# Kernel optimization log

Hardware: AMD Instinct MI355X
Metric: run time of the kernel (lower is better)

The kernel has to match this reference:

```python
import jax, jax.numpy as jnp
import numpy as np

B, T, L = 512, 512, 256
XC, SC, NZ, H, OC = 16, 8, 8, 128, 8
INFO = SC + NZ + 1   # 17: [y, zx, t] channels for the zy (past) encoder
CF = NZ + 1          # 9: [zx, t] channels for the future CDE control
W = 128              # CDEFunc MLP width (width_dfunc default)


def setup_inputs() -> dict:
    key = jax.random.key(0)
    ks = jax.random.split(key, 20)
    rn = lambda k, s: jax.random.normal(k, s, dtype=jnp.float32)
    sc = lambda fan: np.float32(1.0 / np.sqrt(fan))
    return dict(
        y_past=rn(ks[0], (B, L, SC)),
        t=jnp.arange(T, dtype=jnp.float32),
        coeffs_x=rn(ks[1], (B, T, XC)),
        input_length=L,
        zx_wih=rn(ks[2], (3 * H, XC + 1)) * sc(XC + 1),
        zx_whh=rn(ks[3], (3 * H, H)) * sc(H),
        zx_b=rn(ks[4], (3 * H,)) * sc(H),
        zx_bn=rn(ks[5], (H,)) * sc(H),
        zxl_w=rn(ks[6], (NZ, H)) * sc(H),
        zxl_b=rn(ks[7], (NZ,)) * sc(H),
        zy_wih=rn(ks[8], (3 * H, INFO)) * sc(INFO),
        zy_whh=rn(ks[9], (3 * H, H)) * sc(H),
        zy_b=rn(ks[10], (3 * H,)) * sc(H),
        zy_bn=rn(ks[11], (H,)) * sc(H),
        f_w1=rn(ks[12], (W, H)) * sc(H),
        f_b1=rn(ks[13], (W,)) * sc(H),
        f_w2=rn(ks[14], (W, W)) * sc(W),
        f_b2=rn(ks[15], (W,)) * sc(W),
        f_w3=rn(ks[16], (H * CF, W)) * sc(W),
        f_b3=rn(ks[17], (H * CF,)) * sc(W),
        r_w=rn(ks[18], (OC, H)) * sc(H),
        r_b=rn(ks[19], (OC,)) * sc(H),
    )


def _gru(xs, wih, whh, b, bn):
    # xs: (T, B, C). Equinox GRUCell math, batched over B.
    h0 = jnp.zeros((xs.shape[1], whh.shape[1]), xs.dtype)

    def step(h, x):
        i_r, i_z, i_n = jnp.split(x @ wih.T + b, 3, axis=-1)
        g_r, g_z, g_n = jnp.split(h @ whh.T, 3, axis=-1)
        r = jax.nn.sigmoid(i_r + g_r)
        z = jax.nn.sigmoid(i_z + g_z)
        n = jnp.tanh(i_n + r * (g_n + bn))
        hn = n + z * (h - n)  # == new + inp*(hidden-new) in eqx
        return hn, hn

    hT, hs = jax.lax.scan(step, h0, xs)
    return hT, hs


def reference(y_past, t, coeffs_x, input_length,
              zx_wih, zx_whh, zx_b, zx_bn, zxl_w, zxl_b,
              zy_wih, zy_whh, zy_b, zy_bn,
              f_w1, f_b1, f_w2, f_b2, f_w3, f_b3, r_w, r_b):
    Bsz = y_past.shape[0]
    tc = jnp.broadcast_to(t[None, :, None], (Bsz, t.shape[0], 1))
    # --- zx encoder (GRU over control path [X, t]; linear interp at knots == data) ---
    ctrl = jnp.concatenate([coeffs_x, tc], axis=-1)                 # (B,T,XC+1)
    _, hs = _gru(jnp.swapaxes(ctrl, 0, 1), zx_wih, zx_whh, zx_b, zx_bn)
    zx = jnp.swapaxes(hs, 0, 1) @ zxl_w.T + zxl_b                   # (B,T,NZ)
    Lp = input_length
    # --- zy encoder over past control [y, zx, t] (plan_option='full') ---
    ctrl_past = jnp.concatenate([y_past, zx[:, :Lp], tc[:, :Lp]], axis=-1)  # (B,L,INFO)
    zy_current, _ = _gru(jnp.swapaxes(ctrl_past, 0, 1), zy_wih, zy_whh, zy_b, zy_bn)  # (B,H)
    # --- future CDE: dz = f(z) @ dX with linear control X = [zx_future, t_future] ---
    ctrl_fut = jnp.concatenate([zx[:, Lp:], tc[:, Lp:]], axis=-1)   # (B,F,CF)
    dX = jnp.diff(ctrl_fut, axis=1)                                 # (B,F-1,CF)

    def vf(z):  # CDEFunc MLP: (B,H) -> (B,H,CF)
        h1 = jax.nn.softplus(z @ f_w1.T + f_b1)
        h2 = jax.nn.softplus(h1 @ f_w2.T + f_b2)
        o = jnp.tanh(h2 @ f_w3.T + f_b3)
        return o.reshape(z.shape[0], -1, CF)

    def rk4(z, dx):  # one RK4 step per knot interval (dX absorbs dt * slope)
        k1 = jnp.einsum('bhc,bc->bh', vf(z), dx)
        k2 = jnp.einsum('bhc,bc->bh', vf(z + 0.5 * k1), dx)
        k3 = jnp.einsum('bhc,bc->bh', vf(z + 0.5 * k2), dx)
        k4 = jnp.einsum('bhc,bc->bh', vf(z + k3), dx)
        zn = z + (k1 + 2.0 * k2 + 2.0 * k3 + k4) / 6.0
        return zn, zn

    _, zs = jax.lax.scan(rk4, zy_current, jnp.swapaxes(dX, 0, 1))   # (F-1,B,H)
    ys = jnp.concatenate([zy_current[None], zs], axis=0)            # (F,B,H) saveat ts
    y_hat = jnp.swapaxes(ys, 0, 1) @ r_w.T + r_b                    # (B,F,OC)
    return y_hat
```

## Files before the change

### kernel.cpp

```cpp
#include <hip/hip_runtime.h>

#define Bb 512
#define Tt 512
#define Ll 256
#define Ff 256
#define Hh 128
#define H3 384
#define NZ 8
#define XC 16
#define OC 8
#define CF 9
#define W3N 1152
#define BBt 2

__device__ __forceinline__ float sigm(float x){ return 1.0f/(1.0f+expf(-x)); }
__device__ __forceinline__ float softplus_(float x){
  return fmaxf(x, 0.0f) + log1pf(expf(-fabsf(x)));
}
__device__ __forceinline__ float tanh_fast(float x){
  float xc = fminf(fmaxf(x, -9.f), 9.f);
  float e = __expf(2.f*xc);
  return (e - 1.f)/(e + 1.f);
}
__device__ __forceinline__ float dot4(float4 w, float4 z){
  return w.x*z.x + w.y*z.y + w.z*z.z + w.w*z.w;
}
__device__ __forceinline__ int swz32(int i){ return i ^ ((i >> 3) & 3); }
__device__ __forceinline__ int swzf(int h){ return (((h >> 2) ^ ((h >> 5) & 3)) << 2) + (h & 3); }
__device__ __forceinline__ float red4(float p){
  int t;
  t = __builtin_amdgcn_mov_dpp(__builtin_bit_cast(int, p), 0xB1, 0xF, 0xF, true);
  p += __builtin_bit_cast(float, t);
  t = __builtin_amdgcn_mov_dpp(__builtin_bit_cast(int, p), 0x4E, 0xF, 0xF, true);
  p += __builtin_bit_cast(float, t);
  return p;
}
__device__ __forceinline__ float red8(float p){
  p = red4(p);
  int t = __builtin_amdgcn_ds_swizzle(__builtin_bit_cast(int, p), 0x101F);
  p += __builtin_bit_cast(float, t);
  return p;
}

__global__ __launch_bounds__(768) void gru_kernel(
    const float* __restrict__ xin, const float* __restrict__ zx_in,
    const float* __restrict__ tin,
    const float* __restrict__ wih, const float* __restrict__ whh,
    const float* __restrict__ bias, const float* __restrict__ bn,
    const float* __restrict__ zxlw, const float* __restrict__ zxlb,
    float* __restrict__ out_zx, float* __restrict__ out_h,
    int steps, int mode)
{
  const int b = blockIdx.x;
  const int tid = threadIdx.x;
  const int j = tid >> 1;
  const int half = tid & 1;

  float wi[17];
  #pragma unroll
  for (int c = 0; c < 17; c++) wi[c] = wih[j*17 + c];
  const float bj = bias[j];
  float4 wr[16];
  {
    const float4* p = reinterpret_cast<const float4*>(whh + (size_t)j*Hh + half*64);
    #pragma unroll
    for (int q = 0; q < 16; q++) wr[q] = p[q];
  }

  __shared__ __align__(16) float s_h[Hh];
  __shared__ float s_i[H3];
  __shared__ float s_g[H3];
  __shared__ float s_x[17];
  __shared__ float s_bn[Hh];
  __shared__ float s_zxlwT[NZ*Hh];
  __shared__ float s_zxlb[NZ];

  if (tid < Hh){ s_h[tid] = 0.0f; s_bn[tid] = bn[tid]; }
  if (mode == 0){
    for (int q2 = tid; q2 < NZ*Hh; q2 += 768){
      int o = q2 >> 7, rem = q2 & 127, m = rem >> 3, q = rem & 7;
      s_zxlwT[q*128 + o*16 + m] = zxlw[q2];
    }
    if (tid < NZ) s_zxlb[tid] = zxlb[tid];
  }

  float xreg = 0.f;
  if (tid < 17){
    if (mode == 0){
      xreg = (tid < 16) ? xin[(size_t)b*Tt*XC + tid] : tin[0];
    } else {
      if (tid < 8)       xreg = xin[(size_t)b*Ll*NZ + tid];
      else if (tid < 16) xreg = zx_in[(size_t)b*Tt*NZ + (tid - 8)];
      else               xreg = tin[0];
    }
  }
  __syncthreads();

  for (int t = 0; t < steps; t++){
    if (tid < 17) s_x[tid] = xreg;
    __syncthreads();
    float ai = bj;
    #pragma unroll
    for (int c = 0; c < 17; c++) ai += wi[c]*s_x[c];
    float g0=0.f, g1=0.f, g2=0.f, g3=0.f;
    {
      const float4* h4p = reinterpret_cast<const float4*>(&s_h[half*64]);
      #pragma unroll
      for (int q = 0; q < 16; q++){
        float4 w = wr[q];
        float4 h4 = h4p[q];
        g0 += w.x*h4.x; g1 += w.y*h4.y; g2 += w.z*h4.z; g3 += w.w*h4.w;
      }
    }
    float g = (g0+g1)+(g2+g3);
    g += __shfl_xor(g, 1, 64);
    if (half == 0){ s_i[j] = ai; s_g[j] = g; }
    if (tid < 17 && t + 1 < steps){
      const int tn = t + 1;
      if (mode == 0){
        xreg = (tid < 16) ? xin[(size_t)b*Tt*XC + (size_t)tn*XC + tid] : tin[tn];
      } else {
        if (tid < 8)       xreg = xin[(size_t)b*Ll*NZ + (size_t)tn*NZ + tid];
        else if (tid < 16) xreg = zx_in[(size_t)b*Tt*NZ + (size_t)tn*NZ + (tid - 8)];
        else               xreg = tin[tn];
      }
    }
    __syncthreads();
    if (tid < Hh){
      float r  = sigm(s_i[tid]       + s_g[tid]);
      float zz = sigm(s_i[Hh + tid]  + s_g[Hh + tid]);
      float n  = tanhf(s_i[2*Hh+tid] + r*(s_g[2*Hh+tid] + s_bn[tid]));
      s_h[tid] = n + zz*(s_h[tid] - n);
    }
    __syncthreads();
    if (mode == 0){
      if (tid < Hh){
        int m = tid & 15;
        const float4* hp = reinterpret_cast<const float4*>(&s_h[m*8]);
        float4 ha = hp[0], hb = hp[1];
        float p = s_zxlwT[0*128 + tid]*ha.x + s_zxlwT[1*128 + tid]*ha.y
                + s_zxlwT[2*128 + tid]*ha.z + s_zxlwT[3*128 + tid]*ha.w
                + s_zxlwT[4*128 + tid]*hb.x + s_zxlwT[5*128 + tid]*hb.y
                + s_zxlwT[6*128 + tid]*hb.z + s_zxlwT[7*128 + tid]*hb.w;
        p += __shfl_xor(p, 1, 64); p += __shfl_xor(p, 2, 64);
        p += __shfl_xor(p, 4, 64); p += __shfl_xor(p, 8, 64);
        if (m == 0)
          out_zx[(size_t)b*Tt*NZ + (size_t)t*NZ + (tid >> 4)] = s_zxlb[tid >> 4] + p;
      }
    }
  }
  if (mode == 1 && tid < Hh) out_h[b*Hh + tid] = s_h[tid];
}

__global__ __launch_bounds__(512)
__attribute__((amdgpu_waves_per_eu(2, 2)))
void cde_fp32_kernel(
    const float* __restrict__ zy_h, const float* __restrict__ zx,
    const float* __restrict__ tin,
    const float* __restrict__ fw1, const float* __restrict__ fb1,
    const float* __restrict__ fw2, const float* __restrict__ fb2,
    const float* __restrict__ fw3, const float* __restrict__ fb3,
    const float* __restrict__ rw,  const float* __restrict__ rb,
    float* __restrict__ yout)
{
  const int tid = threadIdx.x;
  const int c12 = tid >> 2;
  const int q4  = tid & 3;
  const int col64 = tid >> 3;
  const int e8    = tid & 7;
  const int bg = blockIdx.x * BBt;

  __shared__ __align__(16) float4 s_w1v[4096];
  __shared__ __align__(16) float4 s_w2v[4096];
  __shared__ __align__(16) float4 s_zinv[BBt][32];
  __shared__ __align__(16) float4 s_h1v[BBt][32];
  __shared__ __align__(16) float4 s_h2v[BBt][32];
  __shared__ float s_o[BBt][W3N];
  __shared__ float s_z[BBt][Hh];
  __shared__ float s_kacc[BBt][Hh];
  __shared__ float s_dx[BBt][CF];
  __shared__ float s_rw[OC*Hh];
  __shared__ float s_rb[OC];
  __shared__ float s_b3[W3N];

  float* zin_f0 = reinterpret_cast<float*>(&s_zinv[0][0]);
  float* zin_f1 = reinterpret_cast<float*>(&s_zinv[1][0]);
  float* h1_f0  = reinterpret_cast<float*>(&s_h1v[0][0]);
  float* h1_f1  = reinterpret_cast<float*>(&s_h1v[1][0]);
  float* h2_f0  = reinterpret_cast<float*>(&s_h2v[0][0]);
  float* h2_f1  = reinterpret_cast<float*>(&s_h2v[1][0]);

  for (int idx = tid; idx < Hh*32; idx += 512){
    int col = idx >> 5, jcol = idx & 31;
    int q = jcol >> 3, jj = jcol & 7;
    int dst = jj*512 + col*4 + q;
    s_w1v[dst] = reinterpret_cast<const float4*>(fw1)[idx];
    s_w2v[dst] = reinterpret_cast<const float4*>(fw2)[idx];
  }
  const float b1r = fb1[c12], b2r = fb2[c12];
  for (int idx = tid; idx < W3N; idx += 512) s_b3[idx] = fb3[idx];
  for (int idx = tid; idx < OC*Hh; idx += 512) s_rw[idx] = rw[idx];
  if (tid < OC) s_rb[tid] = rb[tid];
  if (tid < BBt*Hh){
    int b = tid >> 7, h = tid & 127;
    float zv = zy_h[(size_t)(bg + b)*Hh + h];
    s_z[b][h] = zv;
    (b == 0 ? zin_f0 : zin_f1)[swzf(h)] = zv;
  }
  __syncthreads();

  if (tid < 256){
    int b = tid >> 7, r = tid & 127, o = r >> 4, seg = r & 15;
    float p = 0.f;
    #pragma unroll
    for (int q = 0; q < 8; q++)
      p += s_z[b][seg*8 + q]*s_rw[o*Hh + seg*8 + q];
    p += __shfl_xor(p, 1, 64); p += __shfl_xor(p, 2, 64);
    p += __shfl_xor(p, 4, 64); p += __shfl_xor(p, 8, 64);
    if (seg == 0) yout[(size_t)(bg + b)*Ff*OC + o] = s_rb[o] + p;
  }

  const float* w3p = fw3 + (size_t)col64*Hh + e8*16;

  for (int i = 0; i < Ff - 1; i++){
    if (tid < BBt*CF){
      int b = tid/CF, c = tid%CF;
      float d;
      if (c < 8){
        const float* zp = zx + (size_t)(bg + b)*Tt*NZ + (size_t)(Ll + i)*NZ + c;
        d = zp[NZ] - zp[0];
      } else {
        d = tin[Ll + i + 1] - tin[Ll + i];
      }
      s_dx[b][c] = d;
    }
    __syncthreads();

    for (int st = 0; st < 4; st++){
      float4 A0, A1, A2, A3, B0, B1, B2, B3;
      {
        const float4* pA = reinterpret_cast<const float4*>(w3p);
        const float4* pB = reinterpret_cast<const float4*>(w3p + 8192);
        A0 = pA[0]; A1 = pA[1]; A2 = pA[2]; A3 = pA[3];
        B0 = pB[0]; B1 = pB[1]; B2 = pB[2]; B3 = pB[3];
      }
      {
        float p0 = 0.f, p1 = 0.f;
        #pragma unroll
        for (int jj = 0; jj < 8; jj++){
          float4 z0 = s_zinv[0][swz32(q4*8 + jj)];
          float4 z1 = s_zinv[1][swz32(q4*8 + jj)];
          float4 w = s_w1v[jj*512 + tid];
          p0 += dot4(w, z0); p1 += dot4(w, z1);
        }
        p0 = red4(p0); p1 = red4(p1);
        if (q4 == 0){
          h1_f0[swzf(c12)] = softplus_(b1r + p0);
          h1_f1[swzf(c12)] = softplus_(b1r + p1);
        }
      }
      __syncthreads();
      {
        float p0 = 0.f, p1 = 0.f;
        #pragma unroll
        for (int jj = 0; jj < 8; jj++){
          float4 z0 = s_h1v[0][swz32(q4*8 + jj)];
          float4 z1 = s_h1v[1][swz32(q4*8 + jj)];
          float4 w = s_w2v[jj*512 + tid];
          p0 += dot4(w, z0); p1 += dot4(w, z1);
        }
        p0 = red4(p0); p1 = red4(p1);
        if (q4 == 0){
          h2_f0[swzf(c12)] = softplus_(b2r + p0);
          h2_f1[swzf(c12)] = softplus_(b2r + p1);
        }
      }
      __syncthreads();
      {
        float4 h2a0 = s_h2v[0][swz32(e8*4 + 0)];
        float4 h2a1 = s_h2v[0][swz32(e8*4 + 1)];
        float4 h2a2 = s_h2v[0][swz32(e8*4 + 2)];
        float4 h2a3 = s_h2v[0][swz32(e8*4 + 3)];
        float4 h2b0 = s_h2v[1][swz32(e8*4 + 0)];
        float4 h2b1 = s_h2v[1][swz32(e8*4 + 1)];
        float4 h2b2 = s_h2v[1][swz32(e8*4 + 2)];
        float4 h2b3 = s_h2v[1][swz32(e8*4 + 3)];
        #pragma unroll 2
        for (int g = 0; g < 18; g++){
          float4 c0, c1, c2, c3;
          if ((g & 1) == 0){
            c0 = A0; c1 = A1; c2 = A2; c3 = A3;
            if (g + 2 < 18){
              const float4* pF = reinterpret_cast<const float4*>(w3p + (size_t)(g+2)*8192);
              A0 = pF[0]; A1 = pF[1]; A2 = pF[2]; A3 = pF[3];
            }
          } else {
            c0 = B0; c1 = B1; c2 = B2; c3 = B3;
            if (g + 2 < 18){
              const float4* pF = reinterpret_cast<const float4*>(w3p + (size_t)(g+2)*8192);
              B0 = pF[0]; B1 = pF[1]; B2 = pF[2]; B3 = pF[3];
            }
          }
          float p0 = dot4(c0, h2a0) + dot4(c1, h2a1) + dot4(c2, h2a2) + dot4(c3, h2a3);
          float p1 = dot4(c0, h2b0) + dot4(c1, h2b1) + dot4(c2, h2b2) + dot4(c3, h2b3);
          p0 = red8(p0); p1 = red8(p1);
          if (e8 == 0){
            int n = g*64 + col64;
            s_o[0][n] = s_b3[n] + p0;
            s_o[1][n] = s_b3[n] + p1;
          }
        }
      }
      __syncthreads();
      {
        int pr = tid >> 1, hf = tid & 1;
        int b = pr >> 7, h = pr & 127;
        const float* ob = &s_o[0][0] + b*W3N + h*CF;
        float kc = 0.f;
        #pragma unroll
        for (int jj = 0; jj < 4; jj++){
          int c = hf*4 + jj;
          kc += tanh_fast(ob[c]) * s_dx[b][c];
        }
        if (hf) kc += tanh_fast(ob[8]) * s_dx[b][8];
        kc += __shfl_xor(kc, 1, 64);
        if (hf == 0){
          float zv = s_z[b][h], zin;
          if      (st == 0){ s_kacc[b][h] = kc;        zin = zv + 0.5f*kc; }
          else if (st == 1){ s_kacc[b][h] += 2.f*kc;   zin = zv + 0.5f*kc; }
          else if (st == 2){ s_kacc[b][h] += 2.f*kc;   zin = zv + kc; }
          else { float zn = zv + (s_kacc[b][h] + kc)*(1.f/6.f); s_z[b][h] = zn; zin = zn; }
          (b == 0 ? zin_f0 : zin_f1)[swzf(h)] = zin;
        }
      }
      __syncthreads();
    }
    if (tid < 256){
      int b = tid >> 7, r = tid & 127, o = r >> 4, seg = r & 15;
      float p = 0.f;
      #pragma unroll
      for (int q = 0; q < 8; q++)
        p += s_z[b][seg*8 + q]*s_rw[o*Hh + seg*8 + q];
      p += __shfl_xor(p, 1, 64); p += __shfl_xor(p, 2, 64);
      p += __shfl_xor(p, 4, 64); p += __shfl_xor(p, 8, 64);
      if (seg == 0) yout[(size_t)(bg + b)*Ff*OC + (size_t)(i + 1)*OC + o] = s_rb[o] + p;
    }
  }
}

extern "C" void kernel_launch(void* const* d_in, const int* in_sizes, int n_in,
                              void* d_out, int out_size, void* d_ws, size_t ws_size,
                              hipStream_t stream)
{
  (void)in_sizes; (void)n_in; (void)out_size; (void)ws_size;
  const float* y_past = (const float*)d_in[0];
  const float* t_in   = (const float*)d_in[1];
  const float* coeffs = (const float*)d_in[2];
  const float* zx_wih = (const float*)d_in[4];
  const float* zx_whh = (const float*)d_in[5];
  const float* zx_b   = (const float*)d_in[6];
  const float* zx_bn  = (const float*)d_in[7];
  const float* zxl_w  = (const float*)d_in[8];
  const float* zxl_b  = (const float*)d_in[9];
  const float* zy_wih = (const float*)d_in[10];
  const float* zy_whh = (const float*)d_in[11];
  const float* zy_b   = (const float*)d_in[12];
  const float* zy_bn  = (const float*)d_in[13];
  const float* fw1 = (const float*)d_in[14];
  const float* fb1 = (const float*)d_in[15];
  const float* fw2 = (const float*)d_in[16];
  const float* fb2 = (const float*)d_in[17];
  const float* fw3 = (const float*)d_in[18];
  const float* fb3 = (const float*)d_in[19];
  const float* r_w = (const float*)d_in[20];
  const float* r_b = (const float*)d_in[21];

  float* ws = (float*)d_ws;
  float* zx_buf = ws;
  float* zy_buf = ws + (size_t)Bb*Tt*NZ;

  gru_kernel<<<Bb, 768, 0, stream>>>(coeffs, nullptr, t_in,
                                     zx_wih, zx_whh, zx_b, zx_bn,
                                     zxl_w, zxl_b, zx_buf, nullptr, Tt, 0);
  gru_kernel<<<Bb, 768, 0, stream>>>(y_past, zx_buf, t_in,
                                     zy_wih, zy_whh, zy_b, zy_bn,
                                     nullptr, nullptr, nullptr, zy_buf, Ll, 1);
  cde_fp32_kernel<<<Bb/BBt, 512, 0, stream>>>(zy_buf, zx_buf, t_in,
                                              fw1, fb1, fw2, fb2, fw3, fb3,
                                              r_w, r_b, (float*)d_out);
}
```

Measured before the change: 13.54 ms.

## Fuse zx and zy GRU encoders into one kernel and use fast transcendentals

Merges the two GRU launches into a single kernel per batch row. The zx projections for the past window stay in shared memory and feed the zy GRU directly, so they are no longer written to and re-read from global memory. Only the future part of zx still goes to the workspace. Sigmoid, tanh and softplus in the GRU and CDE MLP now use __expf/__logf-based fast versions, which cuts latency on the serial recurrence at some cost in accuracy. The fused kernel uses more shared memory (an extra 8 KB buffer).

Result: faster. 12.00 ms (-11.4%).

```diff
diff --git a/kernel.cpp b/kernel.cpp
--- a/kernel.cpp
+++ b/kernel.cpp
@@ -13,9 +13,10 @@
 #define W3N 1152
 #define BBt 2
 
-__device__ __forceinline__ float sigm(float x){ return 1.0f/(1.0f+expf(-x)); }
-__device__ __forceinline__ float softplus_(float x){
-  return fmaxf(x, 0.0f) + log1pf(expf(-fabsf(x)));
+__device__ __forceinline__ float sigm_fast(float x){ return 1.0f/(1.0f + __expf(-x)); }
+__device__ __forceinline__ float softplus_fast(float x){
+  float u = __expf(-fabsf(x));
+  return fmaxf(x, 0.0f) + __logf(1.0f + u);
 }
 __device__ __forceinline__ float tanh_fast(float x){
   float xc = fminf(fmaxf(x, -9.f), 9.f);
@@ -42,30 +43,20 @@
   return p;
 }
 
-__global__ __launch_bounds__(768) void gru_kernel(
-    const float* __restrict__ xin, const float* __restrict__ zx_in,
+__global__ __launch_bounds__(768) void gru_fused_kernel(
+    const float* __restrict__ coeffs, const float* __restrict__ y_past,
     const float* __restrict__ tin,
-    const float* __restrict__ wih, const float* __restrict__ whh,
-    const float* __restrict__ bias, const float* __restrict__ bn,
-    const float* __restrict__ zxlw, const float* __restrict__ zxlb,
-    float* __restrict__ out_zx, float* __restrict__ out_h,
-    int steps, int mode)
+    const float* __restrict__ zx_wih, const float* __restrict__ zx_whh,
+    const float* __restrict__ zx_b,   const float* __restrict__ zx_bn,
+    const float* __restrict__ zxlw,   const float* __restrict__ zxlb,
+    const float* __restrict__ zy_wih, const float* __restrict__ zy_whh,
+    const float* __restrict__ zy_b,   const float* __restrict__ zy_bn,
+    float* __restrict__ out_zx, float* __restrict__ out_h)
 {
   const int b = blockIdx.x;
   const int tid = threadIdx.x;
   const int j = tid >> 1;
   const int half = tid & 1;
-
-  float wi[17];
-  #pragma unroll
-  for (int c = 0; c < 17; c++) wi[c] = wih[j*17 + c];
-  const float bj = bias[j];
-  float4 wr[16];
-  {
-    const float4* p = reinterpret_cast<const float4*>(whh + (size_t)j*Hh + half*64);
-    #pragma unroll
-    for (int q = 0; q < 16; q++) wr[q] = p[q];
-  }
 
   __shared__ __align__(16) float s_h[Hh];
   __shared__ float s_i[H3];
@@ -74,66 +65,63 @@
   __shared__ float s_bn[Hh];
   __shared__ float s_zxlwT[NZ*Hh];
   __shared__ float s_zxlb[NZ];
-
-  if (tid < Hh){ s_h[tid] = 0.0f; s_bn[tid] = bn[tid]; }
-  if (mode == 0){
+  __shared__ float s_zxh[Ll][NZ];
+
+  {
+    float wi[17];
+    #pragma unroll
+    for (int c = 0; c < 17; c++) wi[c] = zx_wih[j*17 + c];
+    const float bj = zx_b[j];
+    float4 wr[16];
+    {
+      const float4* p = reinterpret_cast<const float4*>(zx_whh + (size_t)j*Hh + half*64);
+      #pragma unroll
+      for (int q = 0; q < 16; q++) wr[q] = p[q];
+    }
+
+    if (tid < Hh){ s_h[tid] = 0.0f; s_bn[tid] = zx_bn[tid]; }
     for (int q2 = tid; q2 < NZ*Hh; q2 += 768){
       int o = q2 >> 7, rem = q2 & 127, m = rem >> 3, q = rem & 7;
       s_zxlwT[q*128 + o*16 + m] = zxlw[q2];
     }
     if (tid < NZ) s_zxlb[tid] = zxlb[tid];
-  }
-
-  float xreg = 0.f;
-  if (tid < 17){
-    if (mode == 0){
-      xreg = (tid < 16) ? xin[(size_t)b*Tt*XC + tid] : tin[0];
-    } else {
-      if (tid < 8)       xreg = xin[(size_t)b*Ll*NZ + tid];
-      else if (tid < 16) xreg = zx_in[(size_t)b*Tt*NZ + (tid - 8)];
-      else               xreg = tin[0];
-    }
-  }
-  __syncthreads();
-
-  for (int t = 0; t < steps; t++){
-    if (tid < 17) s_x[tid] = xreg;
+
+    float xreg = 0.f;
+    if (tid < 17)
+      xreg = (tid < 16) ? coeffs[(size_t)b*Tt*XC + tid] : tin[0];
     __syncthreads();
-    float ai = bj;
-    #pragma unroll
-    for (int c = 0; c < 17; c++) ai += wi[c]*s_x[c];
-    float g0=0.f, g1=0.f, g2=0.f, g3=0.f;
-    {
-      const float4* h4p = reinterpret_cast<const float4*>(&s_h[half*64]);
+
+    for (int t = 0; t < Tt; t++){
+      if (tid < 17) s_x[tid] = xreg;
+      __syncthreads();
+      float ai = bj;
       #pragma unroll
-      for (int q = 0; q < 16; q++){
-        float4 w = wr[q];
-        float4 h4 = h4p[q];
-        g0 += w.x*h4.x; g1 += w.y*h4.y; g2 += w.z*h4.z; g3 += w.w*h4.w;
-      }
-    }
-    float g = (g0+g1)+(g2+g3);
-    g += __shfl_xor(g, 1, 64);
-    if (half == 0){ s_i[j] = ai; s_g[j] = g; }
-    if (tid < 17 && t + 1 < steps){
-      const int tn = t + 1;
-      if (mode == 0){
-        xreg = (tid < 16) ? xin[(size_t)b*Tt*XC + (size_t)tn*XC + tid] : tin[tn];
-      } else {
-        if (tid < 8)       xreg = xin[(size_t)b*Ll*NZ + (size_t)tn*NZ + tid];
-        else if (tid < 16) xreg = zx_in[(size_t)b*Tt*NZ + (size_t)tn*NZ + (tid - 8)];
-        else               xreg = tin[tn];
-      }
-    }
-    __syncthreads();
-    if (tid < Hh){
-      float r  = sigm(s_i[tid]       + s_g[tid]);
-      float zz = sigm(s_i[Hh + tid]  + s_g[Hh + tid]);
-      float n  = tanhf(s_i[2*Hh+tid] + r*(s_g[2*Hh+tid] + s_bn[tid]));
-      s_h[tid] = n + zz*(s_h[tid] - n);
-    }
-    __syncthreads();
-    if (mode == 0){
+      for (int c = 0; c < 17; c++) ai += wi[c]*s_x[c];
+      float g0=0.f, g1=0.f, g2=0.f, g3=0.f;
+      {
+        const float4* h4p = reinterpret_cast<const float4*>(&s_h[half*64]);
+        #pragma unroll
+        for (int q = 0; q < 16; q++){
+          float4 w = wr[q];
+          float4 h4 = h4p[q];
+          g0 += w.x*h4.x; g1 += w.y*h4.y; g2 += w.z*h4.z; g3 += w.w*h4.w;
+        }
+      }
+      float g = (g0+g1)+(g2+g3);
+      g += __shfl_xor(g, 1, 64);
+      if (half == 0){ s_i[j] = ai; s_g[j] = g; }
+      if (tid < 17 && t + 1 < Tt){
+        const int tn = t + 1;
+        xreg = (tid < 16) ? coeffs[(size_t)b*Tt*XC + (size_t)tn*XC + tid] : tin[tn];
+      }
+      __syncthreads();
+      if (tid < Hh){
+        float r  = sigm_fast(s_i[tid]       + s_g[tid]);
+        float zz = sigm_fast(s_i[Hh + tid]  + s_g[Hh + tid]);
+        float n  = tanh_fast(s_i[2*Hh+tid] + r*(s_g[2*Hh+tid] + s_bn[tid]));
+        s_h[tid] = n + zz*(s_h[tid] - n);
+      }
+      __syncthreads();
       if (tid < Hh){
         int m = tid & 15;
         const float4* hp = reinterpret_cast<const float4*>(&s_h[m*8]);
@@ -144,12 +132,71 @@
                 + s_zxlwT[6*128 + tid]*hb.z + s_zxlwT[7*128 + tid]*hb.w;
         p += __shfl_xor(p, 1, 64); p += __shfl_xor(p, 2, 64);
         p += __shfl_xor(p, 4, 64); p += __shfl_xor(p, 8, 64);
-        if (m == 0)
-          out_zx[(size_t)b*Tt*NZ + (size_t)t*NZ + (tid >> 4)] = s_zxlb[tid >> 4] + p;
-      }
-    }
-  }
-  if (mode == 1 && tid < Hh) out_h[b*Hh + tid] = s_h[tid];
+        if (m == 0){
+          int o = tid >> 4;
+          float val = s_zxlb[o] + p;
+          if (t < Ll) s_zxh[t][o] = val;
+          else out_zx[(size_t)b*Tt*NZ + (size_t)t*NZ + o] = val;
+        }
+      }
+    }
+  }
+  __syncthreads();
+
+  {
+    float wi[17];
+    #pragma unroll
+    for (int c = 0; c < 17; c++) wi[c] = zy_wih[j*17 + c];
+    const float bj = zy_b[j];
+    float4 wr[16];
+    {
+      const float4* p = reinterpret_cast<const float4*>(zy_whh + (size_t)j*Hh + half*64);
+      #pragma unroll
+      for (int q = 0; q < 16; q++) wr[q] = p[q];
+    }
+    if (tid < Hh){ s_h[tid] = 0.0f; s_bn[tid] = zy_bn[tid]; }
+
+    float xreg = 0.f;
+    if (tid < 8)        xreg = y_past[(size_t)b*Ll*NZ + tid];
+    else if (tid == 16) xreg = tin[0];
+    __syncthreads();
+
+    for (int t = 0; t < Ll; t++){
+      if (tid < 8)        s_x[tid] = xreg;
+      else if (tid < 16)  s_x[tid] = s_zxh[t][tid - 8];
+      else if (tid == 16) s_x[16] = xreg;
+      __syncthreads();
+      float ai = bj;
+      #pragma unroll
+      for (int c = 0; c < 17; c++) ai += wi[c]*s_x[c];
+      float g0=0.f, g1=0.f, g2=0.f, g3=0.f;
+      {
+        const float4* h4p = reinterpret_cast<const float4*>(&s_h[half*64]);
+        #pragma unroll
+        for (int q = 0; q < 16; q++){
+          float4 w = wr[q];
+          float4 h4 = h4p[q];
+          g0 += w.x*h4.x; g1 += w.y*h4.y; g2 += w.z*h4.z; g3 += w.w*h4.w;
+        }
+      }
+      float g = (g0+g1)+(g2+g3);
+      g += __shfl_xor(g, 1, 64);
+      if (half == 0){ s_i[j] = ai; s_g[j] = g; }
+      if (t + 1 < Ll){
+        if (tid < 8)        xreg = y_past[(size_t)b*Ll*NZ + (size_t)(t+1)*NZ + tid];
+        else if (tid == 16) xreg = tin[t+1];
+      }
+      __syncthreads();
+      if (tid < Hh){
+        float r  = sigm_fast(s_i[tid]       + s_g[tid]);
+        float zz = sigm_fast(s_i[Hh + tid]  + s_g[Hh + tid]);
+        float n  = tanh_fast(s_i[2*Hh+tid] + r*(s_g[2*Hh+tid] + s_bn[tid]));
+        s_h[tid] = n + zz*(s_h[tid] - n);
+      }
+      __syncthreads();
+    }
+    if (tid < Hh) out_h[b*Hh + tid] = s_h[tid];
+  }
 }
 
 __global__ __launch_bounds__(512)
@@ -255,8 +302,8 @@
         }
         p0 = red4(p0); p1 = red4(p1);
         if (q4 == 0){
-          h1_f0[swzf(c12)] = softplus_(b1r + p0);
-          h1_f1[swzf(c12)] = softplus_(b1r + p1);
+          h1_f0[swzf(c12)] = softplus_fast(b1r + p0);
+          h1_f1[swzf(c12)] = softplus_fast(b1r + p1);
         }
       }
       __syncthreads();
@@ -271,8 +318,8 @@
         }
         p0 = red4(p0); p1 = red4(p1);
         if (q4 == 0){
-          h2_f0[swzf(c12)] = softplus_(b2r + p0);
-          h2_f1[swzf(c12)] = softplus_(b2r + p1);
+          h2_f0[swzf(c12)] = softplus_fast(b2r + p0);
+          h2_f1[swzf(c12)] = softplus_fast(b2r + p1);
         }
       }
       __syncthreads();
@@ -379,12 +426,11 @@
   float* zx_buf = ws;
   float* zy_buf = ws + (size_t)Bb*Tt*NZ;
 
-  gru_kernel<<<Bb, 768, 0, stream>>>(coeffs, nullptr, t_in,
-                                     zx_wih, zx_whh, zx_b, zx_bn,
-                                     zxl_w, zxl_b, zx_buf, nullptr, Tt, 0);
-  gru_kernel<<<Bb, 768, 0, stream>>>(y_past, zx_buf, t_in,
-                                     zy_wih, zy_whh, zy_b, zy_bn,
-                                     nullptr, nullptr, nullptr, zy_buf, Ll, 1);
+  gru_fused_kernel<<<Bb, 768, 0, stream>>>(coeffs, y_past, t_in,
+                                           zx_wih, zx_whh, zx_b, zx_bn,
+                                           zxl_w, zxl_b,
+                                           zy_wih, zy_whh, zy_b, zy_bn,
+                                           zx_buf, zy_buf);
   cde_fp32_kernel<<<Bb/BBt, 512, 0, stream>>>(zy_buf, zx_buf, t_in,
                                               fw1, fb1, fw2, fb2, fw3, fb3,
                                               r_w, r_b, (float*)d_out);
```
